# Performance work log

Measured on AMD Instinct MI355X. Metric: run time of the kernel, lower is better.

Reference implementation:

```python
import jax, jax.numpy as jnp
import numpy as np

DIM = 128   # channels
K = 3       # kernel_size
SP = 8      # share_planes
RADIX = 2
B, H, W = 8, 96, 96


def _conv1x1(x, w, b=None):
    # w: (O, I); torch Conv2d 1x1 weight (O, I, 1, 1) squeezed
    y = jnp.einsum('bchw,oc->bohw', x, w)
    return y if b is None else y + b[None, :, None, None]


def _groupnorm(x, g, beta, num_groups, eps=1e-5):
    b, c, h, w = x.shape
    xr = x.reshape(b, num_groups, c // num_groups, h, w)
    m = xr.mean(axis=(2, 3, 4), keepdims=True)
    v = xr.var(axis=(2, 3, 4), keepdims=True)
    xr = (xr - m) / jnp.sqrt(v + eps)
    return xr.reshape(b, c, h, w) * g[None, :, None, None] + beta[None, :, None, None]


def _batchnorm(x, g, beta, eps=1e-5):
    # torch BatchNorm2d in training mode: batch statistics over (B, H, W)
    m = x.mean(axis=(0, 2, 3), keepdims=True)
    v = x.var(axis=(0, 2, 3), keepdims=True)
    return (x - m) / jnp.sqrt(v + eps) * g[None, :, None, None] + beta[None, :, None, None]


def _unfold(x, k):
    # im2col with same padding -> (b, c, k*k, h, w)
    p = (k - 1) // 2
    b, c, h, w = x.shape
    xp = jnp.pad(x, ((0, 0), (0, 0), (p, p), (p, p)))
    pats = [xp[:, :, i:i + h, j:j + w] for i in range(k) for j in range(k)]
    return jnp.stack(pats, axis=2)


def _forward(x, key_w, e_w1, e_w2, e_b2, gn_g, gn_b, c1_w, bn_g, bn_b, se_w1, se_b1, se_w2, se_b2):
    # key_embed: grouped 3x3 conv (groups=4), no bias, ReLU
    k = jax.lax.conv_general_dilated(
        x, key_w, (1, 1), [(K // 2, K // 2)] * 2,
        feature_group_count=4,
        dimension_numbers=('NCHW', 'OIHW', 'NCHW'))
    k = jax.nn.relu(k)
    qk = jnp.concatenate([x, k], axis=1)  # (B, 2*DIM, H, W)
    # embed branch: per-pixel dynamic kernels
    w = jax.nn.relu(_conv1x1(qk, e_w1))
    w = _conv1x1(w, e_w2, e_b2)                    # (B, K*K*DIM//SP, H, W)
    w = _groupnorm(w, gn_g, gn_b, num_groups=DIM // SP)
    b_, _, hh, ww = w.shape
    w = w.reshape(b_, DIM // SP, K * K, hh, ww)    # view(b,1,-1,k*k,h,w)
    # value path + local convolution (per-pixel kernel, shared over SP channels)
    v = _conv1x1(x, c1_w)
    vu = _unfold(v, K).reshape(b_, DIM // SP, SP, K * K, hh, ww)
    y = (vu * w[:, :, None]).sum(axis=3).reshape(b_, DIM, hh, ww)
    y = _batchnorm(y, bn_g, bn_b)
    y = y * jax.nn.sigmoid(y)  # swish
    # radix-softmax SE attention over {y, k}
    xs = jnp.stack([y, k], axis=2)                 # (B, C, radix, H, W)
    gap = xs.sum(axis=2).mean(axis=(2, 3), keepdims=True)  # (B, C, 1, 1)
    a = jax.nn.relu(_conv1x1(gap, se_w1, se_b1))
    a = _conv1x1(a, se_w2, se_b2)                  # (B, radix*C, 1, 1)
    a = jax.nn.softmax(a.reshape(b_, DIM, RADIX), axis=2)
    out = (xs * a[:, :, :, None, None]).sum(axis=2)
    return out


def setup_inputs():
    key = jax.random.key(0)
    ks = jax.random.split(key, 8)
    s = 0.05
    attn_chs = max(DIM * RADIX // 4, 32)  # 64
    wc = K * K * DIM // SP                # 144
    return {
        'x': jax.random.normal(ks[0], (B, DIM, H, W), jnp.float32),
        'key_w': jax.random.normal(ks[1], (DIM, DIM // 4, K, K), jnp.float32) * s,
        'e_w1': jax.random.normal(ks[2], (DIM // 2, 2 * DIM), jnp.float32) * s,
        'e_w2': jax.random.normal(ks[3], (wc, DIM // 2), jnp.float32) * s,
        'e_b2': jnp.zeros((wc,), jnp.float32),
        'gn_g': jnp.ones((wc,), jnp.float32),
        'gn_b': jnp.zeros((wc,), jnp.float32),
        'c1_w': jax.random.normal(ks[4], (DIM, DIM), jnp.float32) * s,
        'bn_g': jnp.ones((DIM,), jnp.float32),
        'bn_b': jnp.zeros((DIM,), jnp.float32),
        'se_w1': jax.random.normal(ks[5], (attn_chs, DIM), jnp.float32) * s,
        'se_b1': jnp.zeros((attn_chs,), jnp.float32),
        'se_w2': jax.random.normal(ks[6], (RADIX * DIM, attn_chs), jnp.float32) * s,
        'se_b2': jnp.zeros((RADIX * DIM,), jnp.float32),
    }


def reference(x, key_w, e_w1, e_w2, e_b2, gn_g, gn_b, c1_w, bn_g, bn_b, se_w1, se_b1, se_w2, se_b2):
    return _forward(x, key_w, e_w1, e_w2, e_b2, gn_g, gn_b, c1_w, bn_g, bn_b,
                    se_w1, se_b1, se_w2, se_b2)
```

## Files before the change

### kernel.cpp

```cpp
#include <hip/hip_runtime.h>
#include <hip/hip_bf16.h>

#define BD 8
#define CD 128
#define HD 96
#define WD 96
#define HW (HD*WD)
#define NPIX (BD*HW)
#define NTOT ((size_t)BD*CD*HW)
#define WC 144
#define NG 16
#define KWRE_OFF 37617664

typedef __hip_bfloat16 bf16;
typedef __attribute__((ext_vector_type(8))) short s8v;
typedef __attribute__((ext_vector_type(4))) float f4v;
typedef __attribute__((ext_vector_type(4))) short s4vv;

__device__ __forceinline__ float b2f(bf16 v){ return __bfloat162float(v); }
__device__ __forceinline__ bf16  f2b(float v){ return __float2bfloat16(v); }
__device__ __forceinline__ short f2bs(float f){ union{ bf16 h; short s; } u; u.h = f2b(f); return u.s; }
__device__ __forceinline__ float bs2f(short s){ union{ bf16 h; short s; } u; u.s = s; return b2f(u.h); }

struct TensPtrs { const void* p[14]; };

__device__ __constant__ int dNelem[14] = {
    9437184, 36864, 16384, 9216, 144, 144, 144, 16384, 128, 128, 8192, 64, 16384, 256
};
__device__ __constant__ int dCanonOff[14] = {
    0, 0, 36864, 53248, 62464, 62608, 62752, 62896, 79280, 79408, 79536, 87728, 87792, 104176
};
__device__ __constant__ int dBOff[14] = {
    -1, 0, 36864, 53248, -1, -1, -1, 62464, -1, -1, -1, -1, -1, -1
};
#define CO_EB2  62464
#define CO_GNG  62608
#define CO_GNB  62752
#define CO_BNG  79280
#define CO_BNB  79408
#define CO_SW1  79536
#define CO_SB1  87728
#define CO_SW2  87792
#define CO_SB2  104176
#define BO_KW   0
#define BO_EW1  36864
#define BO_EW2  53248
#define BO_C1W  62464

__device__ __forceinline__ char* qk_sw(short* base, int px, int e){
    return (char*)base + ((((px*136 + e)*2)) ^ (((px>>3)&7)<<4));
}
__device__ __forceinline__ char* xt_sw(short* base, int px, int e){
    return (char*)base + (((px*32 + e)*2) ^ (((px>>3)&7)<<4));
}

__global__ void k_detect(TensPtrs tp, int* __restrict__ flags){
    int i = blockIdx.x; int tid = threadIdx.x;
    int n = dNelem[i];
    int m = n < 4096 ? n : 4096;
    int pairs = m >> 1;
    const unsigned int* u = (const unsigned int*)tp.p[i];
    int v = 0;
    for (int j = tid; j < pairs; j += 256){
        unsigned int w = u[j];
        unsigned short lo = (unsigned short)(w & 0xffff);
        unsigned short hi = (unsigned short)(w >> 16);
        int e = (lo >> 7) & 0xFF;
        bool wild = (e >= 0xBE) || (e > 0 && e < 0x40);
        if (wild || (lo == 0 && hi != 0)) v++;
    }
    __shared__ int sv[256];
    sv[tid] = v; __syncthreads();
    for (int st = 128; st > 0; st >>= 1){
        if (tid < st) sv[tid] += sv[tid+st];
        __syncthreads();
    }
    if (tid == 0) flags[i] = (sv[0]*8 > pairs) ? 1 : 0;
}

__global__ void k_canon(TensPtrs tp, const int* __restrict__ flags,
                        float* __restrict__ canonf, short* __restrict__ canonb){
    int i = (blockIdx.x >> 4) + 1;
    int chunk = blockIdx.x & 15;
    int n = dNelem[i]; int off = dCanonOff[i]; int bo = dBOff[i];
    bool f32 = flags[i] != 0;
    for (int j = chunk*256 + threadIdx.x; j < n; j += 4096){
        float v = f32 ? ((const float*)tp.p[i])[j] : b2f(((const bf16*)tp.p[i])[j]);
        canonf[off + j] = v;
        if (bo >= 0) canonb[bo + j] = f2bs(v);
    }
}

__global__ void k_xcast(const void* __restrict__ x, const int* __restrict__ flags,
                        unsigned short* __restrict__ xb){
    int blk = blockIdx.x;
    size_t i = ((size_t)((blk & 7)*1152 + (blk >> 3)))*256 + threadIdx.x;
    if (flags[0]){
        float4 v = ((const float4*)x)[i];
        ushort4 o;
        o.x = (unsigned short)f2bs(v.x); o.y = (unsigned short)f2bs(v.y);
        o.z = (unsigned short)f2bs(v.z); o.w = (unsigned short)f2bs(v.w);
        ((ushort4*)xb)[i] = o;
    } else {
        ((ushort4*)xb)[i] = ((const ushort4*)x)[i];
    }
}

__global__ void k_reorder_kw(const short* __restrict__ canonb, short* __restrict__ kwre){
    int idx = blockIdx.x*256 + threadIdx.x;
    if (idx >= 36864) return;
    int g = idx / 9216, rem = idx - g*9216;
    int oc = rem / 288, r2 = rem - oc*288;
    int ic = r2 / 9, t = r2 - ic*9;
    kwre[g*9216 + t*1024 + oc*32 + ic] = canonb[BO_KW + idx];
}

__global__ void k_zero(float* __restrict__ p, int n){
    int i = blockIdx.x*256 + threadIdx.x;
    if (i < n) p[i] = 0.f;
}

__global__ void k_keyconv_mfma(const short* __restrict__ xb,
                               const short* __restrict__ kwre, bf16* __restrict__ kout){
    __shared__ short xt[588*32];
    int blk = blockIdx.x;
    int b = blk & 7, j = blk >> 3;
    int band = j % 24, g = j / 24;
    int r0 = band*4;
    int tid = threadIdx.x;
    for (int idx = tid; idx < 1152; idx += 256){
        int pr = idx / 192, rem = idx - pr*192;
        int c2 = rem / 12, gx = rem - c2*12;
        int ir = r0 - 1 + pr;
        int c = c2*2;
        s8v t0 = (s8v){0,0,0,0,0,0,0,0};
        s8v t1 = (s8v){0,0,0,0,0,0,0,0};
        if ((unsigned)ir < 96u){
            size_t gb = ((size_t)b*CD + g*32 + c)*HW + (size_t)ir*WD + gx*8;
            t0 = *(const s8v*)(xb + gb);
            t1 = *(const s8v*)(xb + gb + HW);
        }
        #pragma unroll
        for (int jj = 0; jj < 8; ++jj){
            int pxl = pr*98 + gx*8 + 1 + jj;
            unsigned int pk = (unsigned int)(unsigned short)t0[jj]
                            | ((unsigned int)(unsigned short)t1[jj] << 16);
            *(unsigned int*)xt_sw(xt, pxl, c) = pk;
        }
    }
    for (int idx = tid; idx < 192; idx += 256){
        int pr = idx / 32, rem = idx - pr*32;
        int e = rem >> 4, c2 = rem & 15;
        int pxl = pr*98 + (e ? 97 : 0);
        *(unsigned int*)xt_sw(xt, pxl, c2*2) = 0u;
    }
    __syncthreads();
    int wave = tid >> 6, lane = tid & 63, l15 = lane & 15, quad = lane >> 4;
    f4v acc[2][6];
    #pragma unroll
    for (int m = 0; m < 2; ++m)
        #pragma unroll
        for (int n = 0; n < 6; ++n) acc[m][n] = (f4v){0.f,0.f,0.f,0.f};
    const short* kg = kwre + g*9216;
    for (int t = 0; t < 9; ++t){
        s8v A0 = *(const s8v*)(kg + t*1024 + l15*32 + quad*8);
        s8v A1 = *(const s8v*)(kg + t*1024 + (16+l15)*32 + quad*8);
        int pbase = (wave + t/3)*98 + (t%3) + l15;
        #pragma unroll
        for (int n = 0; n < 6; ++n){
            int pxl = pbase + n*16;
            s8v B = *(const s8v*)xt_sw(xt, pxl, quad*8);
            acc[0][n] = __builtin_amdgcn_mfma_f32_16x16x32_bf16(A0, B, acc[0][n], 0, 0, 0);
            acc[1][n] = __builtin_amdgcn_mfma_f32_16x16x32_bf16(A1, B, acc[1][n], 0, 0, 0);
        }
    }
    int r = r0 + wave;
    #pragma unroll
    for (int m = 0; m < 2; ++m)
        #pragma unroll
        for (int n = 0; n < 6; ++n)
            #pragma unroll
            for (int reg = 0; reg < 4; ++reg){
                int oc = g*32 + m*16 + quad*4 + reg;
                int px = n*16 + l15;
                kout[((size_t)b*CD + oc)*HW + r*WD + px] = f2b(fmaxf(acc[m][n][reg], 0.f));
            }
}

__global__ void k_vconv_mfma(const void* __restrict__ x, const int* __restrict__ flags,
                             const short* __restrict__ c1wb, bf16* __restrict__ vout){
    __shared__ short xt[96*136];
    int blk = blockIdx.x; int b = blk / 96, r = blk % 96;
    int tid = threadIdx.x;
    bool F = flags[0] != 0;
    for (int idx = tid; idx < 1536; idx += 256){
        int oct = idx / 96, px = idx - oct*96;
        size_t base = ((size_t)b*CD + oct*8)*HW + r*WD + px;
        s8v tmp;
        #pragma unroll
        for (int j = 0; j < 8; ++j){
            float v = F ? ((const float*)x)[base + (size_t)j*HW]
                        : b2f(((const bf16*)x)[base + (size_t)j*HW]);
            tmp[j] = f2bs(v);
        }
        *(s8v*)(xt + px*136 + oct*8) = tmp;
    }
    __syncthreads();
    int wave = tid >> 6, lane = tid & 63, l15 = lane & 15, quad = lane >> 4;
    f4v acc[2][6];
    #pragma unroll
    for (int m = 0; m < 2; ++m)
        #pragma unroll
        for (int n = 0; n < 6; ++n) acc[m][n] = (f4v){0.f,0.f,0.f,0.f};
    for (int k0 = 0; k0 < 128; k0 += 32){
        s8v Bf[6];
        #pragma unroll
        for (int n = 0; n < 6; ++n) Bf[n] = *(const s8v*)(xt + (n*16+l15)*136 + k0 + quad*8);
        #pragma unroll
        for (int m = 0; m < 2; ++m){
            int oc0 = (wave*2 + m)*16;
            s8v A = *(const s8v*)(c1wb + BO_C1W + (oc0 + l15)*128 + k0 + quad*8);
            #pragma unroll
            for (int n = 0; n < 6; ++n)
                acc[m][n] = __builtin_amdgcn_mfma_f32_16x16x32_bf16(A, Bf[n], acc[m][n], 0, 0, 0);
        }
    }
    #pragma unroll
    for (int m = 0; m < 2; ++m)
        #pragma unroll
        for (int n = 0; n < 6; ++n)
            #pragma unroll
            for (int reg = 0; reg < 4; ++reg){
                int oc = (wave*2+m)*16 + quad*4 + reg;
                int px = n*16 + l15;
                vout[((size_t)b*CD + oc)*HW + r*WD + px] = f2b(acc[m][n][reg]);
            }
}

__global__ void k_embed_stats(const short* __restrict__ xb,
                              const bf16* __restrict__ kbuf, const short* __restrict__ canonb,
                              const float* __restrict__ canonf,
                              unsigned short* __restrict__ w1b, bf16* __restrict__ vout,
                              float* __restrict__ gsum_s, float* __restrict__ gsq_s){
    __shared__ short qk[48*136];
    __shared__ short w1s[48*72];
    __shared__ float gacc[16], gacc2[16];
    const short* ew1b = canonb + BO_EW1;
    const short* ew2b = canonb + BO_EW2;
    const float* eb2f = canonf + CO_EB2;
    int blk = blockIdx.x;
    int b = blk & 7, j = blk >> 3;
    int px0 = (j & 1)*48, r = j >> 1;
    int tid = threadIdx.x;
    int wave = tid >> 6, lane = tid & 63, l15 = lane & 15, quad = lane >> 4;
    if (tid < 16){ gacc[tid] = 0.f; gacc2[tid] = 0.f; }
    for (int idx = tid; idx < 384; idx += 256){
        int c2 = idx / 6, p8 = idx - c2*6;
        int c = c2*2;
        size_t gb = ((size_t)b*CD + c)*HW + r*WD + px0 + p8*8;
        s8v t0 = *(const s8v*)(xb + gb);
        s8v t1 = *(const s8v*)(xb + gb + HW);
        #pragma unroll
        for (int jj = 0; jj < 8; ++jj){
            int px = p8*8 + jj;
            unsigned int pk = (unsigned int)(unsigned short)t0[jj]
                            | ((unsigned int)(unsigned short)t1[jj] << 16);
            *(unsigned int*)qk_sw(qk, px, c) = pk;
        }
    }
    __syncthreads();
    f4v a1[3];
    #pragma unroll
    for (int n = 0; n < 3; ++n) a1[n] = (f4v){0.f,0.f,0.f,0.f};
    int mb = wave*16;
    for (int k0 = 0; k0 < 128; k0 += 32){
        s8v A = *(const s8v*)(ew1b + (mb + l15)*256 + k0 + quad*8);
        #pragma unroll
        for (int n = 0; n < 3; ++n){
            int px = n*16 + l15;
            s8v Bf = *(const s8v*)qk_sw(qk, px, k0 + quad*8);
            a1[n] = __builtin_amdgcn_mfma_f32_16x16x32_bf16(A, Bf, a1[n], 0, 0, 0);
        }
    }
    {
        f4v av[2][3];
        #pragma unroll
        for (int m = 0; m < 2; ++m)
            #pragma unroll
            for (int n = 0; n < 3; ++n) av[m][n] = (f4v){0.f,0.f,0.f,0.f};
        for (int k0 = 0; k0 < 128; k0 += 32){
            s8v Bf[3];
            #pragma unroll
            for (int n = 0; n < 3; ++n){
                int px = n*16 + l15;
                Bf[n] = *(const s8v*)qk_sw(qk, px, k0 + quad*8);
            }
            #pragma unroll
            for (int m = 0; m < 2; ++m){
                int oc0 = (wave*2 + m)*16;
                s8v A = *(const s8v*)(canonb + BO_C1W + (oc0 + l15)*128 + k0 + quad*8);
                #pragma unroll
                for (int n = 0; n < 3; ++n)
                    av[m][n] = __builtin_amdgcn_mfma_f32_16x16x32_bf16(A, Bf[n], av[m][n], 0, 0, 0);
            }
        }
        #pragma unroll
        for (int m = 0; m < 2; ++m)
            #pragma unroll
            for (int n = 0; n < 3; ++n)
                #pragma unroll
                for (int reg = 0; reg < 4; ++reg){
                    int oc = (wave*2+m)*16 + quad*4 + reg;
                    int px = n*16 + l15;
                    vout[((size_t)b*CD + oc)*HW + r*WD + px0 + px] = f2b(av[m][n][reg]);
                }
    }
    __syncthreads();
    {
        const short* kb = (const short*)kbuf;
        for (int idx = tid; idx < 384; idx += 256){
            int c2 = idx / 6, p8 = idx - c2*6;
            int c = c2*2;
            size_t gb = ((size_t)b*CD + c)*HW + r*WD + px0 + p8*8;
            s8v t0 = *(const s8v*)(kb + gb);
            s8v t1 = *(const s8v*)(kb + gb + HW);
            #pragma unroll
            for (int jj = 0; jj < 8; ++jj){
                int px = p8*8 + jj;
                unsigned int pk = (unsigned int)(unsigned short)t0[jj]
                                | ((unsigned int)(unsigned short)t1[jj] << 16);
                *(unsigned int*)qk_sw(qk, px, c) = pk;
            }
        }
    }
    __syncthreads();
    for (int k0 = 128; k0 < 256; k0 += 32){
        s8v A = *(const s8v*)(ew1b + (mb + l15)*256 + k0 + quad*8);
        #pragma unroll
        for (int n = 0; n < 3; ++n){
            int px = n*16 + l15;
            s8v Bf = *(const s8v*)qk_sw(qk, px, (k0-128) + quad*8);
            a1[n] = __builtin_amdgcn_mfma_f32_16x16x32_bf16(A, Bf, a1[n], 0, 0, 0);
        }
    }
    #pragma unroll
    for (int n = 0; n < 3; ++n)
        #pragma unroll
        for (int reg = 0; reg < 4; ++reg){
            int ch = mb + quad*4 + reg;
            int px = n*16 + l15;
            w1s[px*72 + ch] = f2bs(fmaxf(a1[n][reg], 0.f));
        }
    __syncthreads();
    size_t gpx0 = (size_t)b*HW + r*WD + px0;
    for (int idx = tid; idx < 768; idx += 256){
        int px = idx >> 4, s4 = idx & 15;
        ushort4 v4 = *(const ushort4*)((const unsigned short*)w1s + px*72 + s4*4);
        *(ushort4*)(w1b + (gpx0 + px)*64 + s4*4) = v4;
    }
    {
        f4v a2[3][3];
        #pragma unroll
        for (int i = 0; i < 3; ++i)
            #pragma unroll
            for (int n = 0; n < 3; ++n) a2[i][n] = (f4v){0.f,0.f,0.f,0.f};
        for (int k0 = 0; k0 < 64; k0 += 32){
            s8v Bf[3];
            #pragma unroll
            for (int n = 0; n < 3; ++n) Bf[n] = *(const s8v*)(w1s + (n*16+l15)*72 + k0 + quad*8);
            #pragma unroll
            for (int i = 0; i < 3; ++i){
                int mt = wave + i*4;
                if (mt >= 9) break;
                s8v A = *(const s8v*)(ew2b + (mt*16 + l15)*64 + k0 + quad*8);
                #pragma unroll
                for (int n = 0; n < 3; ++n)
                    a2[i][n] = __builtin_amdgcn_mfma_f32_16x16x32_bf16(A, Bf[n], a2[i][n], 0, 0, 0);
            }
        }
        #pragma unroll
        for (int i = 0; i < 3; ++i){
            int mt = wave + i*4;
            if (mt >= 9) break;
            #pragma unroll
            for (int n = 0; n < 3; ++n)
                #pragma unroll
                for (int reg = 0; reg < 4; ++reg){
                    int o = mt*16 + quad*4 + reg;
                    float v = a2[i][n][reg] + eb2f[o];
                    float s = v, q = v*v;
                    #pragma unroll
                    for (int off = 1; off < 16; off <<= 1){
                        s += __shfl_xor(s, off);
                        q += __shfl_xor(q, off);
                    }
                    if (l15 == 0){
                        int g = o / 9;
                        atomicAdd(&gacc[g], s);
                        atomicAdd(&gacc2[g], q);
                    }
                }
        }
    }
    __syncthreads();
    if (tid < 16){
        int slot = j & 63;
        atomicAdd(&gsum_s[(b*NG + tid)*64 + slot], gacc[tid]);
        atomicAdd(&gsq_s [(b*NG + tid)*64 + slot], gacc2[tid]);
    }
}

__global__ void k_embed_apply(const unsigned short* __restrict__ w1b,
                              const short* __restrict__ canonb, const float* __restrict__ canonf,
                              const float* __restrict__ gmean, const float* __restrict__ gistd,
                              const bf16* __restrict__ vbuf, float* __restrict__ yout){
    __shared__ short w2s[9216];
    __shared__ short w1s[48*72];
    __shared__ float wsc[WC], wbi[WC];
    const short* ew2b = canonb + BO_EW2;
    const float* eb2f = canonf + CO_EB2;
    int blk = blockIdx.x;
    int b = blk & 7, j = blk >> 3;
    int px0 = (j & 1)*48, r = j >> 1;
    int tid = threadIdx.x;
    int wave = tid >> 6, lane = tid & 63, l15 = lane & 15, quad = lane >> 4;
    if (tid < WC){
        int g = tid/9;
        float m = gmean[b*NG+g], is = gistd[b*NG+g];
        float ga = canonf[CO_GNG + tid], be = canonf[CO_GNB + tid];
        wsc[tid] = is*ga; wbi[tid] = be - m*is*ga;
    }
    size_t gpx0 = (size_t)b*HW + r*WD + px0;
    for (int idx = tid; idx < 768; idx += 256){
        int px = idx >> 4, s4 = idx & 15;
        ushort4 v4 = *(const ushort4*)(w1b + (gpx0 + px)*64 + s4*4);
        *(ushort4*)((unsigned short*)w1s + px*72 + s4*4) = v4;
    }
    __syncthreads();
    {
        f4v a2[3][3];
        #pragma unroll
        for (int i = 0; i < 3; ++i)
            #pragma unroll
            for (int n = 0; n < 3; ++n) a2[i][n] = (f4v){0.f,0.f,0.f,0.f};
        for (int k0 = 0; k0 < 64; k0 += 32){
            s8v Bf[3];
            #pragma unroll
            for (int n = 0; n < 3; ++n) Bf[n] = *(const s8v*)(w1s + (n*16+l15)*72 + k0 + quad*8);
            #pragma unroll
            for (int i = 0; i < 3; ++i){
                int mt = wave + i*4;
                if (mt >= 9) break;
                s8v A = *(const s8v*)(ew2b + (mt*16 + l15)*64 + k0 + quad*8);
                #pragma unroll
                for (int n = 0; n < 3; ++n)
                    a2[i][n] = __builtin_amdgcn_mfma_f32_16x16x32_bf16(A, Bf[n], a2[i][n], 0, 0, 0);
            }
        }
        #pragma unroll
        for (int i = 0; i < 3; ++i){
            int mt = wave + i*4;
            if (mt >= 9) break;
            #pragma unroll
            for (int n = 0; n < 3; ++n)
                #pragma unroll
                for (int reg = 0; reg < 4; ++reg){
                    int o = mt*16 + quad*4 + reg;
                    int px = n*16 + l15;
                    float val = (a2[i][n][reg] + eb2f[o])*wsc[o] + wbi[o];
                    int g = o/9, t = o - g*9;
                    int tr3 = (t >= 3) + (t >= 6);
                    int tc = t - tr3*3;
                    int gcol = px0 + px;
                    bool kill = (r == 0 && tr3 == 0) || (r == 95 && tr3 == 2)
                             || (gcol == 0 && tc == 0) || (gcol == 95 && tc == 2);
                    w2s[g*576 + px*12 + t] = kill ? (short)0 : f2bs(val);
                }
        }
    }
    __syncthreads();
    const short* vb = (const short*)vbuf;
    long base0 = (long)b*CD*HW + (long)(r - 1)*WD + (px0 - 1);
    for (int it = tid; it < 6144; it += 256){
        int c = it / 48, px = it - c*48;
        const short* wp = w2s + (c>>3)*576 + px*12;
        s4vv wA = *(const s4vv*)wp;
        s4vv wB = *(const s4vv*)(wp + 4);
        float w8 = bs2f(wp[8]);
        const short* vp = vb + base0 + (long)c*HW + px;
        float acc;
        acc  = bs2f(vp[0])   * bs2f(wA[0]);
        acc += bs2f(vp[1])   * bs2f(wA[1]);
        acc += bs2f(vp[2])   * bs2f(wA[2]);
        acc += bs2f(vp[96])  * bs2f(wA[3]);
        acc += bs2f(vp[97])  * bs2f(wB[0]);
        acc += bs2f(vp[98])  * bs2f(wB[1]);
        acc += bs2f(vp[192]) * bs2f(wB[2]);
        acc += bs2f(vp[193]) * bs2f(wB[3]);
        acc += bs2f(vp[194]) * w8;
        yout[((size_t)b*CD + c)*HW + (size_t)r*WD + px0 + px] = acc;
    }
}

__global__ void k_bnstat(const float* __restrict__ y, float* __restrict__ bnsum_s,
                         float* __restrict__ bnss_s){
    int blk = blockIdx.x;
    int c = blk >> 3, slice = blk & 7;
    int tid = threadIdx.x;
    const float4* y4 = (const float4*)y;
    float s = 0.f, ss = 0.f;
    int i0 = slice*2304;
    for (int k = 0; k < 9; ++k){
        int i = i0 + k*256 + tid;
        int b = i / 2304, p4 = i - b*2304;
        float4 v = y4[(size_t)(b*CD + c)*2304 + p4];
        s += v.x + v.y + v.z + v.w;
        ss += v.x*v.x + v.y*v.y + v.z*v.z + v.w*v.w;
    }
    __shared__ float sh[256], sh2[256];
    sh[tid] = s; sh2[tid] = ss;
    __syncthreads();
    for (int st = 128; st > 0; st >>= 1){
        if (tid < st){ sh[tid] += sh[tid+st]; sh2[tid] += sh2[tid+st]; }
        __syncthreads();
    }
    if (tid == 0){
        bnsum_s[c*256 + slice] = sh[0];
        bnss_s [c*256 + slice] = sh2[0];
    }
}

template<bool APPLY>
__global__ void k_embed_mfma(const void* __restrict__ x, const int* __restrict__ flags,
                             const bf16* __restrict__ kbuf, const short* __restrict__ canonb,
                             const float* __restrict__ canonf,
                             const float* __restrict__ gmean, const float* __restrict__ gistd,
                             const bf16* __restrict__ vbuf, float* __restrict__ yout,
                             float* __restrict__ gsum_s, float* __restrict__ gsq_s,
                             float* __restrict__ bnsum_s, float* __restrict__ bnss_s){
    __shared__ char buf0[26624];
    __shared__ short w1s[48*72];
    __shared__ short w2s[48*152];
    __shared__ float wsc[WC], wbi[WC];
    __shared__ float blks[256], blkq[256];
    short* qk = (short*)buf0;
    float* yt = (float*)buf0;
    const short* ew1b = canonb + BO_EW1;
    const short* ew2b = canonb + BO_EW2;
    const float* eb2f = canonf + CO_EB2;
    int blk = blockIdx.x;
    int px0 = (blk & 1)*48, r = (blk >> 1) % 96, b = blk / 192;
    int tid = threadIdx.x;
    bool F = flags[0] != 0;
    if (APPLY && tid < WC){
        int g = tid/9;
        float m = gmean[b*NG+g], is = gistd[b*NG+g];
        float ga = canonf[CO_GNG + tid], be = canonf[CO_GNB + tid];
        wsc[tid] = is*ga; wbi[tid] = be - m*is*ga;
    }
    for (int idx = tid; idx < 128*48; idx += 256){
        int c = idx / 48, px = idx - c*48;
        size_t off = ((size_t)b*CD + c)*HW + r*WD + px0 + px;
        float v = F ? ((const float*)x)[off] : b2f(((const bf16*)x)[off]);
        qk[px*264 + c] = f2bs(v);
    }
    for (int idx = tid; idx < 128*48; idx += 256){
        int c = idx / 48, px = idx - c*48;
        qk[px*264 + 128 + c] = ((const short*)kbuf)[((size_t)b*CD + c)*HW + r*WD + px0 + px];
    }
    __syncthreads();
    int wave = tid >> 6, lane = tid & 63, l15 = lane & 15, quad = lane >> 4;
    {
        f4v a1[3];
        #pragma unroll
        for (int n = 0; n < 3; ++n) a1[n] = (f4v){0.f,0.f,0.f,0.f};
        int mb = wave*16;
        for (int k0 = 0; k0 < 256; k0 += 32){
            s8v A = *(const s8v*)(ew1b + (mb + l15)*256 + k0 + quad*8);
            #pragma unroll
            for (int n = 0; n < 3; ++n){
                s8v Bf = *(const s8v*)(qk + (n*16+l15)*264 + k0 + quad*8);
                a1[n] = __builtin_amdgcn_mfma_f32_16x16x32_bf16(A, Bf, a1[n], 0, 0, 0);
            }
        }
        __syncthreads();
        #pragma unroll
        for (int n = 0; n < 3; ++n)
            #pragma unroll
            for (int reg = 0; reg < 4; ++reg){
                int ch = mb + quad*4 + reg;
                int px = n*16 + l15;
                w1s[px*72 + ch] = f2bs(fmaxf(a1[n][reg], 0.f));
            }
    }
    __syncthreads();
    {
        f4v a2[3][3];
        #pragma unroll
        for (int i = 0; i < 3; ++i)
            #pragma unroll
            for (int n = 0; n < 3; ++n) a2[i][n] = (f4v){0.f,0.f,0.f,0.f};
        for (int k0 = 0; k0 < 64; k0 += 32){
            s8v Bf[3];
            #pragma unroll
            for (int n = 0; n < 3; ++n) Bf[n] = *(const s8v*)(w1s + (n*16+l15)*72 + k0 + quad*8);
            #pragma unroll
            for (int i = 0; i < 3; ++i){
                int mt = wave + i*4;
                if (mt >= 9) break;
                s8v A = *(const s8v*)(ew2b + (mt*16 + l15)*64 + k0 + quad*8);
                #pragma unroll
                for (int n = 0; n < 3; ++n)
                    a2[i][n] = __builtin_amdgcn_mfma_f32_16x16x32_bf16(A, Bf[n], a2[i][n], 0, 0, 0);
            }
        }
        #pragma unroll
        for (int i = 0; i < 3; ++i){
            int mt = wave + i*4;
            if (mt >= 9) break;
            #pragma unroll
            for (int n = 0; n < 3; ++n)
                #pragma unroll
                for (int reg = 0; reg < 4; ++reg){
                    int o = mt*16 + quad*4 + reg;
                    int px = n*16 + l15;
                    float val = a2[i][n][reg] + eb2f[o];
                    if (APPLY) val = val*wsc[o] + wbi[o];
                    w2s[px*152 + o] = f2bs(val);
                }
        }
    }
    __syncthreads();
    if (!APPLY){
        if (tid < WC){
            int o = tid; float s = 0.f, ss = 0.f;
            for (int px = 0; px < 48; ++px){ float v = bs2f(w2s[px*152+o]); s += v; ss += v*v; }
            int g = o/9; int slot = blk & 63;
            atomicAdd(&gsum_s[(b*NG+g)*64 + slot], s);
            atomicAdd(&gsq_s [(b*NG+g)*64 + slot], ss);
        }
        return;
    }
    if (tid < 192){
        int px = tid % 48, cq = tid / 48;
        int gcol = px0 + px;
        for (int c = cq*32; c < cq*32 + 32; ++c){
            int g9 = (c >> 3)*9;
            const bf16* vb = vbuf + ((size_t)b*CD + c)*HW;
            float acc = 0.f;
            #pragma unroll
            for (int t = 0; t < 9; ++t){
                int ir = r + t/3 - 1, icc = gcol + t%3 - 1;
                if ((unsigned)ir < 96u && (unsigned)icc < 96u)
                    acc += b2f(vb[ir*WD + icc]) * bs2f(w2s[px*152 + g9 + t]);
            }
            yt[c*52 + px] = acc;
        }
    }
    __syncthreads();
    {
        int c = tid & 127, half = tid >> 7;
        float s = 0.f, ss = 0.f;
        for (int px = half*24; px < half*24 + 24; ++px){
            float v = yt[c*52 + px]; s += v; ss += v*v;
        }
        blks[tid] = s; blkq[tid] = ss;
    }
    __syncthreads();
    if (tid < 128){
        float s = blks[tid] + blks[tid+128];
        float ss = blkq[tid] + blkq[tid+128];
        int slot = blk & 255;
        atomicAdd(&bnsum_s[tid*256 + slot], s);
        atomicAdd(&bnss_s [tid*256 + slot], ss);
    }
    for (int idx = tid; idx < 128*48; idx += 256){
        int c = idx / 48, px = idx - c*48;
        yout[((size_t)b*CD + c)*HW + r*WD + px0 + px] = yt[c*52 + px];
    }
}

__global__ void k_gnfin(const float* __restrict__ gsum_s, const float* __restrict__ gsq_s,
                        float* __restrict__ gmean, float* __restrict__ gistd){
    int i = threadIdx.x;
    float s = 0.f, ss = 0.f;
    for (int k = 0; k < 64; ++k){ s += gsum_s[i*64 + k]; ss += gsq_s[i*64 + k]; }
    float inv = 1.f / (9.f*HW);
    float m = s*inv;
    float var = ss*inv - m*m;
    gmean[i] = m;
    gistd[i] = rsqrtf(var + 1e-5f);
}

__global__ void k_bnfin(const float* __restrict__ bnsum_s, const float* __restrict__ bnss_s,
                        const float* __restrict__ canonf,
                        float* __restrict__ scale, float* __restrict__ shift){
    int c = threadIdx.x;
    float s = 0.f, ss = 0.f;
    for (int k = 0; k < 256; ++k){ s += bnsum_s[c*256 + k]; ss += bnss_s[c*256 + k]; }
    float inv = 1.f / (float)(BD*HW);
    float m = s*inv;
    float var = ss*inv - m*m;
    float sc = canonf[CO_BNG + c] * rsqrtf(var + 1e-5f);
    scale[c] = sc;
    shift[c] = canonf[CO_BNB + c] - m*sc;
}

__global__ void k_gap(const float* __restrict__ ybuf, const bf16* __restrict__ kbuf,
                      const float* __restrict__ scale, const float* __restrict__ shift,
                      float* __restrict__ gap){
    int blk = blockIdx.x;
    int bc = (blk & 7)*CD + (blk >> 3);
    int c = bc % CD;
    int tid = threadIdx.x;
    float sc = scale[c], sh = shift[c];
    const float4* y4 = (const float4*)ybuf + (size_t)bc*2304;
    const ushort4* k4 = (const ushort4*)kbuf + (size_t)bc*2304;
    float gs = 0.f;
    for (int k = 0; k < 9; ++k){
        int i = k*256 + tid;
        float4 yv = y4[i];
        ushort4 kv = k4[i];
        #pragma unroll
        for (int j = 0; j < 4; ++j){
            float yn = ((&yv.x)[j])*sc + sh;
            float ys = yn / (1.f + __expf(-yn));
            gs += ys + bs2f((short)((&kv.x)[j]));
        }
    }
    __shared__ float shm[256];
    shm[tid] = gs; __syncthreads();
    for (int st = 128; st > 0; st >>= 1){
        if (tid < st) shm[tid] += shm[tid+st];
        __syncthreads();
    }
    if (tid == 0) gap[bc] = shm[0];
}

__global__ void k_se(const float* __restrict__ gap, const float* __restrict__ canonf,
                     float* __restrict__ p0, float* __restrict__ p1){
    int b = blockIdx.x;
    int tid = threadIdx.x;
    __shared__ float loc[128], h1[64];
    float invhw = 1.f / (float)HW;
    loc[tid]      = gap[b*CD + tid]      * invhw;
    loc[tid + 64] = gap[b*CD + tid + 64] * invhw;
    __syncthreads();
    {
        const float* wr = canonf + CO_SW1 + (size_t)tid*128;
        float acc = canonf[CO_SB1 + tid];
        for (int c = 0; c < 128; ++c) acc += wr[c] * loc[c];
        h1[tid] = fmaxf(acc, 0.f);
    }
    __syncthreads();
    for (int c = tid; c < 128; c += 64){
        float a0 = canonf[CO_SB2 + 2*c], a1 = canonf[CO_SB2 + 2*c+1];
        const float* w0 = canonf + CO_SW2 + (size_t)(2*c)*64;
        const float* w1p = canonf + CO_SW2 + (size_t)(2*c+1)*64;
        for (int j = 0; j < 64; ++j){
            a0 += w0[j] * h1[j];
            a1 += w1p[j] * h1[j];
        }
        float mx = fmaxf(a0, a1);
        float e0 = __expf(a0-mx), e1 = __expf(a1-mx);
        float inv = 1.f / (e0 + e1);
        p0[b*CD+c] = e0*inv;
        p1[b*CD+c] = e1*inv;
    }
}

__global__ void k_out(float* __restrict__ ybuf, const bf16* __restrict__ kbuf,
                      const float* __restrict__ scale, const float* __restrict__ shift,
                      const float* __restrict__ p0, const float* __restrict__ p1){
    int blk = blockIdx.x;
    size_t idx = ((size_t)((blk & 7)*1152 + (blk >> 3)))*256 + threadIdx.x;
    int bc = (int)(idx / 2304);
    int c = bc % CD;
    float sc = scale[c], sh = shift[c];
    float q0 = p0[bc], q1 = p1[bc];
    float4 yv = ((const float4*)ybuf)[idx];
    ushort4 kv = ((const ushort4*)kbuf)[idx];
    float4 ov;
    #pragma unroll
    for (int j = 0; j < 4; ++j){
        float yn = ((&yv.x)[j])*sc + sh;
        float ys = yn / (1.f + __expf(-yn));
        (&ov.x)[j] = ys*q0 + bs2f((short)((&kv.x)[j]))*q1;
    }
    ((float4*)ybuf)[idx] = ov;
}

extern "C" void kernel_launch(void* const* d_in, const int* in_sizes, int n_in,
                              void* d_out, int out_size, void* d_ws, size_t ws_size,
                              hipStream_t stream) {
    TensPtrs tp;
    for (int i = 0; i < 14; ++i) tp.p[i] = d_in[i];

    float* f = (float*)d_ws;
    float* bnsum_s = f;
    float* bnss_s  = f + 32768;
    float* gsum_s  = f + 65536;
    float* gsq_s   = f + 73728;
    float* gap     = f + 81920;
    float* gmean   = f + 82944;
    float* gistd   = f + 83072;
    float* bscale  = f + 83200;
    float* bshift  = f + 83328;
    float* p0      = f + 83456;
    float* p1      = f + 84480;
    int*   flags = (int*)((char*)d_ws + 393216);
    float* canonf = (float*)((char*)d_ws + 425984);
    short* canonb = (short*)((char*)d_ws + 860160);
    bf16*  kbuf  = (bf16*)((char*)d_ws + 1048576);
    bf16*  vbuf  = kbuf + NTOT;
    unsigned short* w1b = (unsigned short*)((char*)d_ws + 38797312);
    float* ybuf  = (float*)d_out;
    short* kwre = (short*)((char*)d_out + KWRE_OFF);
    unsigned short* xb16 = (unsigned short*)d_out;

    bool fast = ws_size >= 48234496ull;

    k_detect<<<14, 256, 0, stream>>>(tp, flags);
    k_canon<<<208, 256, 0, stream>>>(tp, flags, canonf, canonb);
    k_xcast<<<(int)(NTOT/4/256), 256, 0, stream>>>(d_in[0], flags, xb16);
    k_reorder_kw<<<144, 256, 0, stream>>>(canonb, kwre);
    k_zero<<<324, 256, 0, stream>>>(f, 82944);
    k_keyconv_mfma<<<768, 256, 0, stream>>>((const short*)xb16, kwre, kbuf);
    if (fast){
        k_embed_stats<<<1536, 256, 0, stream>>>((const short*)xb16, kbuf, canonb, canonf,
                                                w1b, vbuf, gsum_s, gsq_s);
        k_gnfin<<<1, 128, 0, stream>>>(gsum_s, gsq_s, gmean, gistd);
        k_embed_apply<<<1536, 256, 0, stream>>>(w1b, canonb, canonf, gmean, gistd,
                                                vbuf, ybuf);
        k_bnstat<<<1024, 256, 0, stream>>>(ybuf, bnsum_s, bnss_s);
    } else {
        k_embed_mfma<false><<<1536, 256, 0, stream>>>(d_in[0], flags, kbuf, canonb, canonf,
                                                      gmean, gistd, vbuf, ybuf,
                                                      gsum_s, gsq_s, bnsum_s, bnss_s);
        k_gnfin<<<1, 128, 0, stream>>>(gsum_s, gsq_s, gmean, gistd);
        k_vconv_mfma<<<768, 256, 0, stream>>>(d_in[0], flags, canonb, vbuf);
        k_embed_mfma<true><<<1536, 256, 0, stream>>>(d_in[0], flags, kbuf, canonb, canonf,
                                                     gmean, gistd, vbuf, ybuf,
                                                     gsum_s, gsq_s, bnsum_s, bnss_s);
    }
    k_bnfin<<<1, 128, 0, stream>>>(bnsum_s, bnss_s, canonf, bscale, bshift);
    k_gap<<<1024, 256, 0, stream>>>(ybuf, kbuf, bscale, bshift, gap);
    k_se<<<BD, 64, 0, stream>>>(gap, canonf, p0, p1);
    k_out<<<(int)(NTOT/4/256), 256, 0, stream>>>(ybuf, kbuf, bscale, bshift, p0, p1);
}
```

Baseline: 262.1 us.

## Fuse BN stats and key GAP into producers, skip bf16 input copy

Batch-norm sum and sum-of-squares move into k_embed_apply through shared-memory atomics followed by global atomics, which removes the separate k_bnstat pass over the float output. The key-branch global-average contribution is accumulated inside the key conv with shuffles and atomics, so k_gap no longer reads kbuf. k_xcast now returns early when the input is already bf16, and the consumers read the original input directly instead of a copy. k_embed_stats also loads the x and k tiles together up front. In exchange there is heavy shared-memory atomic contention on 128 channels per block, and gap relies on the zeroing kernel now running before k_xcast.

```diff
diff --git a/kernel.cpp b/kernel.cpp
--- a/kernel.cpp
+++ b/kernel.cpp
@@ -53,6 +53,15 @@
 __device__ __forceinline__ char* xt_sw(short* base, int px, int e){
     return (char*)base + (((px*32 + e)*2) ^ (((px>>3)&7)<<4));
 }
+__device__ __forceinline__ void qk_write(short* qk, int p8, int c, s8v t0, s8v t1){
+    #pragma unroll
+    for (int jj = 0; jj < 8; ++jj){
+        int px = p8*8 + jj;
+        unsigned int pk = (unsigned int)(unsigned short)t0[jj]
+                        | ((unsigned int)(unsigned short)t1[jj] << 16);
+        *(unsigned int*)qk_sw(qk, px, c) = pk;
+    }
+}
 
 __global__ void k_detect(TensPtrs tp, int* __restrict__ flags){
     int i = blockIdx.x; int tid = threadIdx.x;
@@ -93,16 +102,16 @@
 
 __global__ void k_xcast(const void* __restrict__ x, const int* __restrict__ flags,
                         unsigned short* __restrict__ xb){
+    if (!flags[0]) return;
     int blk = blockIdx.x;
-    size_t i = ((size_t)((blk & 7)*1152 + (blk >> 3)))*256 + threadIdx.x;
-    if (flags[0]){
+    size_t base = ((size_t)((blk & 7)*128 + (blk >> 3)))*2304;
+    for (int k = 0; k < 9; ++k){
+        size_t i = base + k*256 + threadIdx.x;
         float4 v = ((const float4*)x)[i];
         ushort4 o;
         o.x = (unsigned short)f2bs(v.x); o.y = (unsigned short)f2bs(v.y);
         o.z = (unsigned short)f2bs(v.z); o.w = (unsigned short)f2bs(v.w);
         ((ushort4*)xb)[i] = o;
-    } else {
-        ((ushort4*)xb)[i] = ((const ushort4*)x)[i];
     }
 }
 
@@ -120,14 +129,17 @@
     if (i < n) p[i] = 0.f;
 }
 
-__global__ void k_keyconv_mfma(const short* __restrict__ xb,
-                               const short* __restrict__ kwre, bf16* __restrict__ kout){
+__global__ void k_keyconv_mfma(const short* __restrict__ xb, const short* __restrict__ xorig,
+                               const int* __restrict__ flags,
+                               const short* __restrict__ kwre, bf16* __restrict__ kout,
+                               float* __restrict__ kgap){
     __shared__ short xt[588*32];
     int blk = blockIdx.x;
     int b = blk & 7, j = blk >> 3;
     int band = j % 24, g = j / 24;
     int r0 = band*4;
     int tid = threadIdx.x;
+    const short* xs = flags[0] ? xb : xorig;
     for (int idx = tid; idx < 1152; idx += 256){
         int pr = idx / 192, rem = idx - pr*192;
         int c2 = rem / 12, gx = rem - c2*12;
@@ -137,8 +149,8 @@
         s8v t1 = (s8v){0,0,0,0,0,0,0,0};
         if ((unsigned)ir < 96u){
             size_t gb = ((size_t)b*CD + g*32 + c)*HW + (size_t)ir*WD + gx*8;
-            t0 = *(const s8v*)(xb + gb);
-            t1 = *(const s8v*)(xb + gb + HW);
+            t0 = *(const s8v*)(xs + gb);
+            t1 = *(const s8v*)(xs + gb + HW);
         }
         #pragma unroll
         for (int jj = 0; jj < 8; ++jj){
@@ -185,6 +197,20 @@
                 int px = n*16 + l15;
                 kout[((size_t)b*CD + oc)*HW + r*WD + px] = f2b(fmaxf(acc[m][n][reg], 0.f));
             }
+    #pragma unroll
+    for (int m = 0; m < 2; ++m)
+        #pragma unroll
+        for (int reg = 0; reg < 4; ++reg){
+            float s = 0.f;
+            #pragma unroll
+            for (int n = 0; n < 6; ++n) s += fmaxf(acc[m][n][reg], 0.f);
+            #pragma unroll
+            for (int off = 1; off < 16; off <<= 1) s += __shfl_xor(s, off);
+            if (l15 == 0){
+                int oc = g*32 + m*16 + quad*4 + reg;
+                atomicAdd(&kgap[b*CD + oc], s);
+            }
+        }
 }
 
 __global__ void k_vconv_mfma(const void* __restrict__ x, const int* __restrict__ flags,
@@ -237,7 +263,8 @@
             }
 }
 
-__global__ void k_embed_stats(const short* __restrict__ xb,
+__global__ void k_embed_stats(const short* __restrict__ xb, const short* __restrict__ xorig,
+                              const int* __restrict__ flags,
                               const bf16* __restrict__ kbuf, const short* __restrict__ canonb,
                               const float* __restrict__ canonf,
                               unsigned short* __restrict__ w1b, bf16* __restrict__ vout,
@@ -253,21 +280,28 @@
     int px0 = (j & 1)*48, r = j >> 1;
     int tid = threadIdx.x;
     int wave = tid >> 6, lane = tid & 63, l15 = lane & 15, quad = lane >> 4;
+    const short* xs = flags[0] ? xb : xorig;
+    const short* kb = (const short*)kbuf;
     if (tid < 16){ gacc[tid] = 0.f; gacc2[tid] = 0.f; }
-    for (int idx = tid; idx < 384; idx += 256){
-        int c2 = idx / 6, p8 = idx - c2*6;
-        int c = c2*2;
-        size_t gb = ((size_t)b*CD + c)*HW + r*WD + px0 + p8*8;
-        s8v t0 = *(const s8v*)(xb + gb);
-        s8v t1 = *(const s8v*)(xb + gb + HW);
-        #pragma unroll
-        for (int jj = 0; jj < 8; ++jj){
-            int px = p8*8 + jj;
-            unsigned int pk = (unsigned int)(unsigned short)t0[jj]
-                            | ((unsigned int)(unsigned short)t1[jj] << 16);
-            *(unsigned int*)qk_sw(qk, px, c) = pk;
-        }
-    }
+    int c2a = tid / 6, p8a = tid - c2a*6;
+    size_t gba = ((size_t)b*CD + c2a*2)*HW + r*WD + px0 + p8a*8;
+    bool has2 = tid < 128;
+    int ib = 256 + tid;
+    int c2b = ib / 6, p8b = ib - c2b*6;
+    size_t gbb = ((size_t)b*CD + c2b*2)*HW + r*WD + px0 + p8b*8;
+    s8v xa0 = *(const s8v*)(xs + gba);
+    s8v xa1 = *(const s8v*)(xs + gba + HW);
+    s8v ka0 = *(const s8v*)(kb + gba);
+    s8v ka1 = *(const s8v*)(kb + gba + HW);
+    s8v xb0, xb1, kb0, kb1;
+    if (has2){
+        xb0 = *(const s8v*)(xs + gbb);
+        xb1 = *(const s8v*)(xs + gbb + HW);
+        kb0 = *(const s8v*)(kb + gbb);
+        kb1 = *(const s8v*)(kb + gbb + HW);
+    }
+    qk_write(qk, p8a, c2a*2, xa0, xa1);
+    if (has2) qk_write(qk, p8b, c2b*2, xb0, xb1);
     __syncthreads();
     f4v a1[3];
     #pragma unroll
@@ -316,23 +350,8 @@
                 }
     }
     __syncthreads();
-    {
-        const short* kb = (const short*)kbuf;
-        for (int idx = tid; idx < 384; idx += 256){
-            int c2 = idx / 6, p8 = idx - c2*6;
-            int c = c2*2;
-            size_t gb = ((size_t)b*CD + c)*HW + r*WD + px0 + p8*8;
-            s8v t0 = *(const s8v*)(kb + gb);
-            s8v t1 = *(const s8v*)(kb + gb + HW);
-            #pragma unroll
-            for (int jj = 0; jj < 8; ++jj){
-                int px = p8*8 + jj;
-                unsigned int pk = (unsigned int)(unsigned short)t0[jj]
-                                | ((unsigned int)(unsigned short)t1[jj] << 16);
-                *(unsigned int*)qk_sw(qk, px, c) = pk;
-            }
-        }
-    }
+    qk_write(qk, p8a, c2a*2, ka0, ka1);
+    if (has2) qk_write(qk, p8b, c2b*2, kb0, kb1);
     __syncthreads();
     for (int k0 = 128; k0 < 256; k0 += 32){
         s8v A = *(const s8v*)(ew1b + (mb + l15)*256 + k0 + quad*8);
@@ -413,10 +432,13 @@
 __global__ void k_embed_apply(const unsigned short* __restrict__ w1b,
                               const short* __restrict__ canonb, const float* __restrict__ canonf,
                               const float* __restrict__ gmean, const float* __restrict__ gistd,
-                              const bf16* __restrict__ vbuf, float* __restrict__ yout){
+                              const bf16* __restrict__ vbuf, float* __restrict__ yout,
+                              float* __restrict__ bnsum_s, float* __restrict__ bnss_s){
     __shared__ short w2s[9216];
     __shared__ short w1s[48*72];
     __shared__ float wsc[WC], wbi[WC];
+    float* bns = (float*)w1s;
+    float* bnq = bns + 128;
     const short* ew2b = canonb + BO_EW2;
     const float* eb2f = canonf + CO_EB2;
     int blk = blockIdx.x;
@@ -478,6 +500,8 @@
                 }
         }
     }
+    __syncthreads();
+    if (tid < 128){ bns[tid] = 0.f; bnq[tid] = 0.f; }
     __syncthreads();
     const short* vb = (const short*)vbuf;
     long base0 = (long)b*CD*HW + (long)(r - 1)*WD + (px0 - 1);
@@ -499,34 +523,14 @@
         acc += bs2f(vp[193]) * bs2f(wB[3]);
         acc += bs2f(vp[194]) * w8;
         yout[((size_t)b*CD + c)*HW + (size_t)r*WD + px0 + px] = acc;
-    }
-}
-
-__global__ void k_bnstat(const float* __restrict__ y, float* __restrict__ bnsum_s,
-                         float* __restrict__ bnss_s){
-    int blk = blockIdx.x;
-    int c = blk >> 3, slice = blk & 7;
-    int tid = threadIdx.x;
-    const float4* y4 = (const float4*)y;
-    float s = 0.f, ss = 0.f;
-    int i0 = slice*2304;
-    for (int k = 0; k < 9; ++k){
-        int i = i0 + k*256 + tid;
-        int b = i / 2304, p4 = i - b*2304;
-        float4 v = y4[(size_t)(b*CD + c)*2304 + p4];
-        s += v.x + v.y + v.z + v.w;
-        ss += v.x*v.x + v.y*v.y + v.z*v.z + v.w*v.w;
-    }
-    __shared__ float sh[256], sh2[256];
-    sh[tid] = s; sh2[tid] = ss;
-    __syncthreads();
-    for (int st = 128; st > 0; st >>= 1){
-        if (tid < st){ sh[tid] += sh[tid+st]; sh2[tid] += sh2[tid+st]; }
-        __syncthreads();
-    }
-    if (tid == 0){
-        bnsum_s[c*256 + slice] = sh[0];
-        bnss_s [c*256 + slice] = sh2[0];
+        atomicAdd(&bns[c], acc);
+        atomicAdd(&bnq[c], acc*acc);
+    }
+    __syncthreads();
+    if (tid < 128){
+        int slot = blk & 255;
+        atomicAdd(&bnsum_s[tid*256 + slot], bns[tid]);
+        atomicAdd(&bnss_s [tid*256 + slot], bnq[tid]);
     }
 }
 
@@ -706,7 +710,7 @@
     shift[c] = canonf[CO_BNB + c] - m*sc;
 }
 
-__global__ void k_gap(const float* __restrict__ ybuf, const bf16* __restrict__ kbuf,
+__global__ void k_gap(const float* __restrict__ ybuf,
                       const float* __restrict__ scale, const float* __restrict__ shift,
                       float* __restrict__ gap){
     int blk = blockIdx.x;
@@ -715,17 +719,13 @@
     int tid = threadIdx.x;
     float sc = scale[c], sh = shift[c];
     const float4* y4 = (const float4*)ybuf + (size_t)bc*2304;
-    const ushort4* k4 = (const ushort4*)kbuf + (size_t)bc*2304;
     float gs = 0.f;
     for (int k = 0; k < 9; ++k){
-        int i = k*256 + tid;
-        float4 yv = y4[i];
-        ushort4 kv = k4[i];
+        float4 yv = y4[k*256 + tid];
         #pragma unroll
         for (int j = 0; j < 4; ++j){
             float yn = ((&yv.x)[j])*sc + sh;
-            float ys = yn / (1.f + __expf(-yn));
-            gs += ys + bs2f((short)((&kv.x)[j]));
+            gs += yn / (1.f + __expf(-yn));
         }
     }
     __shared__ float shm[256];
@@ -734,7 +734,7 @@
         if (tid < st) shm[tid] += shm[tid+st];
         __syncthreads();
     }
-    if (tid == 0) gap[bc] = shm[0];
+    if (tid == 0) gap[bc] += shm[0];
 }
 
 __global__ void k_se(const float* __restrict__ gap, const float* __restrict__ canonf,
@@ -822,17 +822,18 @@
 
     k_detect<<<14, 256, 0, stream>>>(tp, flags);
     k_canon<<<208, 256, 0, stream>>>(tp, flags, canonf, canonb);
-    k_xcast<<<(int)(NTOT/4/256), 256, 0, stream>>>(d_in[0], flags, xb16);
+    k_zero<<<324, 256, 0, stream>>>(f, 82944);
+    k_xcast<<<1024, 256, 0, stream>>>(d_in[0], flags, xb16);
     k_reorder_kw<<<144, 256, 0, stream>>>(canonb, kwre);
-    k_zero<<<324, 256, 0, stream>>>(f, 82944);
-    k_keyconv_mfma<<<768, 256, 0, stream>>>((const short*)xb16, kwre, kbuf);
+    k_keyconv_mfma<<<768, 256, 0, stream>>>((const short*)xb16, (const short*)d_in[0],
+                                            flags, kwre, kbuf, gap);
     if (fast){
-        k_embed_stats<<<1536, 256, 0, stream>>>((const short*)xb16, kbuf, canonb, canonf,
+        k_embed_stats<<<1536, 256, 0, stream>>>((const short*)xb16, (const short*)d_in[0],
+                                                flags, kbuf, canonb, canonf,
                                                 w1b, vbuf, gsum_s, gsq_s);
         k_gnfin<<<1, 128, 0, stream>>>(gsum_s, gsq_s, gmean, gistd);
         k_embed_apply<<<1536, 256, 0, stream>>>(w1b, canonb, canonf, gmean, gistd,
-                                                vbuf, ybuf);
-        k_bnstat<<<1024, 256, 0, stream>>>(ybuf, bnsum_s, bnss_s);
+                                                vbuf, ybuf, bnsum_s, bnss_s);
     } else {
         k_embed_mfma<false><<<1536, 256, 0, stream>>>(d_in[0], flags, kbuf, canonb, canonf,
                                                       gmean, gistd, vbuf, ybuf,
@@ -844,7 +845,7 @@
                                                      gsum_s, gsq_s, bnsum_s, bnss_s);
     }
     k_bnfin<<<1, 128, 0, stream>>>(bnsum_s, bnss_s, canonf, bscale, bshift);
-    k_gap<<<1024, 256, 0, stream>>>(ybuf, kbuf, bscale, bshift, gap);
+    k_gap<<<1024, 256, 0, stream>>>(ybuf, bscale, bshift, gap);
     k_se<<<BD, 64, 0, stream>>>(gap, canonf, p0, p1);
     k_out<<<(int)(NTOT/4/256), 256, 0, stream>>>(ybuf, kbuf, bscale, bshift, p0, p1);
 }
```

After: 375.1 us. +43.1%, slower.
